# Kernel tuning notes

Measured on AMD Instinct MI355X. Metric: run time of the kernel, lower is better.

The kernel has to match this reference:

```python
import jax, jax.numpy as jnp
import numpy as np

N = 4096          # nodes (single graph, batch=None)
E = 65536         # edges (avg degree 16)
C = 256           # hidden_channels
L = 3             # num_layers
H = 8             # attention heads
EPS = 1e-5        # batchnorm eps


def setup_inputs() -> dict:
    key = jax.random.key(0)
    ks = iter(jax.random.split(key, 64))
    s = 0.05
    d = {}
    d['x'] = jax.random.normal(next(ks), (N, 1), dtype=jnp.float32)
    d['edge_index'] = jax.random.randint(next(ks), (2, E), 0, N, dtype=jnp.int32)
    # input projection Linear(1, C)
    d['lin1_w'] = jax.random.normal(next(ks), (C, 1), dtype=jnp.float32) * s
    d['lin1_b'] = jnp.zeros((C,), dtype=jnp.float32)
    # GIN MLP: Linear(C,C) -> ReLU -> Linear(C,C), stacked over layers
    d['gin_w1'] = jax.random.normal(next(ks), (L, C, C), dtype=jnp.float32) * s
    d['gin_b1'] = jnp.zeros((L, C), dtype=jnp.float32)
    d['gin_w2'] = jax.random.normal(next(ks), (L, C, C), dtype=jnp.float32) * s
    d['gin_b2'] = jnp.zeros((L, C), dtype=jnp.float32)
    # MultiheadAttention projections
    for nm in ['attn_wq', 'attn_wk', 'attn_wv', 'attn_wo']:
        d[nm] = jax.random.normal(next(ks), (L, C, C), dtype=jnp.float32) * s
    for nm in ['attn_bq', 'attn_bk', 'attn_bv', 'attn_bo']:
        d[nm] = jnp.zeros((L, C), dtype=jnp.float32)
    # three BatchNorms per GPSConv layer
    for nm in ['bn1', 'bn2', 'bn3']:
        d[nm + '_g'] = jnp.ones((L, C), dtype=jnp.float32)
        d[nm + '_b'] = jnp.zeros((L, C), dtype=jnp.float32)
    # GPSConv feedforward: Linear(C, 2C) -> ReLU -> Linear(2C, C)
    d['mlp_w1'] = jax.random.normal(next(ks), (L, 2 * C, C), dtype=jnp.float32) * s
    d['mlp_b1'] = jnp.zeros((L, 2 * C), dtype=jnp.float32)
    d['mlp_w2'] = jax.random.normal(next(ks), (L, C, 2 * C), dtype=jnp.float32) * s
    d['mlp_b2'] = jnp.zeros((L, C), dtype=jnp.float32)
    return d


def _bn(v, g, b):
    # training-mode BatchNorm1d over the node dimension (biased variance)
    m = v.mean(0)
    var = v.var(0)
    return (v - m) * jax.lax.rsqrt(var + EPS) * g + b


def _gps_forward(x, edge_index, lin1_w, lin1_b, gin_w1, gin_b1, gin_w2, gin_b2,
                 attn_wq, attn_bq, attn_wk, attn_bk, attn_wv, attn_bv,
                 attn_wo, attn_bo, bn1_g, bn1_b, bn2_g, bn2_b, bn3_g, bn3_b,
                 mlp_w1, mlp_b1, mlp_w2, mlp_b2):
    h = x @ lin1_w.T + lin1_b                     # [N, C]
    src, dst = edge_index[0], edge_index[1]
    dh = C // H
    scale = 1.0 / jnp.sqrt(jnp.float32(dh))
    for l in range(L):
        xin = h
        # --- GIN branch: gather -> scatter-sum -> MLP ---
        agg = jax.ops.segment_sum(xin[src], dst, num_segments=N)   # [N, C]
        z = xin + agg                                               # eps=0
        z = jax.nn.relu(z @ gin_w1[l].T + gin_b1[l]) @ gin_w2[l].T + gin_b2[l]
        h1 = _bn(z + xin, bn1_g[l], bn1_b[l])
        # --- global multihead attention over all N nodes ---
        q = (xin @ attn_wq[l].T + attn_bq[l]).reshape(N, H, dh)
        k = (xin @ attn_wk[l].T + attn_bk[l]).reshape(N, H, dh)
        v = (xin @ attn_wv[l].T + attn_bv[l]).reshape(N, H, dh)
        scores = jnp.einsum('nhd,mhd->hnm', q, k) * scale           # [H, N, N]
        a = jax.nn.softmax(scores, axis=-1)
        o = jnp.einsum('hnm,mhd->nhd', a, v).reshape(N, C)
        o = o @ attn_wo[l].T + attn_bo[l]
        h2 = _bn(o + xin, bn2_g[l], bn2_b[l])
        # --- combine + feedforward ---
        s = h1 + h2
        m = jax.nn.relu(s @ mlp_w1[l].T + mlp_b1[l]) @ mlp_w2[l].T + mlp_b2[l]
        h = _bn(s + m, bn3_g[l], bn3_b[l])
    return h


def reference(x, edge_index, lin1_w, lin1_b, gin_w1, gin_b1, gin_w2, gin_b2,
              attn_wq, attn_bq, attn_wk, attn_bk, attn_wv, attn_bv,
              attn_wo, attn_bo, bn1_g, bn1_b, bn2_g, bn2_b, bn3_g, bn3_b,
              mlp_w1, mlp_b1, mlp_w2, mlp_b2):
    return _gps_forward(x, edge_index, lin1_w, lin1_b, gin_w1, gin_b1, gin_w2,
                        gin_b2, attn_wq, attn_bq, attn_wk, attn_bk, attn_wv,
                        attn_bv, attn_wo, attn_bo, bn1_g, bn1_b, bn2_g, bn2_b,
                        bn3_g, bn3_b, mlp_w1, mlp_b1, mlp_w2, mlp_b2)
```

## Files before the change

### kernel.cpp

```cpp
#include <hip/hip_runtime.h>

#define NN 4096
#define NE 65536
#define C 256
#define NL 3
#define NH 8
#define DH 32
#define EPS 1e-5f
#define SPLIT 4
#define KT8 (NN/128/SPLIT)
#define QB 256
#define ATTN_BLKS ((NN/QB)*NH*SPLIT)
#define VS 136

typedef __bf16 bf16x8 __attribute__((ext_vector_type(8)));
typedef __bf16 bf16x4v __attribute__((ext_vector_type(4)));
typedef float f32x4 __attribute__((ext_vector_type(4)));
typedef short bf16x4s __attribute__((ext_vector_type(4)));

#define QSCALE (0.17677669529663687f * 1.4426950408889634f)

#define CC1 (C*C)
#define GS 72

__global__ __launch_bounds__(256) void prep_w(const float* __restrict__ s0,
        const float* __restrict__ s1, const float* __restrict__ s2,
        const float* __restrict__ s3, const float* __restrict__ s4,
        const float* __restrict__ s5, const float* __restrict__ s6,
        const float* __restrict__ s7, __bf16* __restrict__ dst) {
    int g = blockIdx.y;
    int i = (blockIdx.x*256 + threadIdx.x)*4;
    const float* src; int n;
    switch (g) {
        case 0: src=s0; n=3*CC1; break;
        case 1: src=s1; n=3*CC1; break;
        case 2: src=s2; n=3*CC1; break;
        case 3: src=s3; n=3*CC1; break;
        case 4: src=s4; n=3*CC1; break;
        case 5: src=s5; n=3*CC1; break;
        case 6: src=s6; n=6*CC1; break;
        default: src=s7; n=6*CC1; break;
    }
    if (i >= n) return;
    size_t off;
    if (g >= 2 && g <= 4) {
        int l = i >> 16, rem = i & (CC1-1);
        off = (size_t)(6 + 3*l + (g-2))*CC1 + rem;
    } else {
        size_t base = (g==0) ? 0 : (g==1) ? 3*(size_t)CC1 : (g==5) ? 15*(size_t)CC1
                    : (g==6) ? 18*(size_t)CC1 : 24*(size_t)CC1;
        off = base + i;
    }
    float4 t = *(const float4*)(src + i);
    bf16x4v o = {(__bf16)t.x, (__bf16)t.y, (__bf16)t.z, (__bf16)t.w};
    *(bf16x4v*)(dst + off) = o;
}

__global__ __launch_bounds__(256) void lin1_kernel(const float* __restrict__ x,
        const float* __restrict__ w, const float* __restrict__ b,
        __bf16* __restrict__ out) {
    int n = blockIdx.x, c = threadIdx.x;
    out[(size_t)n*C + c] = (__bf16)(x[n]*w[c] + b[c]);
}

__global__ __launch_bounds__(256) void hist_kernel(const int* __restrict__ ei,
        int* __restrict__ cnt) {
    int e = blockIdx.x*256 + threadIdx.x;
    atomicAdd(&cnt[ei[NE + e]], 1);
}

__global__ __launch_bounds__(256) void scan_kernel(const int* __restrict__ cnt,
        int* __restrict__ rowptr, int* __restrict__ cursor) {
    __shared__ int tot[256];
    __shared__ int pre[257];
    int t = threadIdx.x;
    int base = t*16;
    int local[16];
    int s = 0;
    #pragma unroll
    for (int i = 0; i < 16; i++) { local[i] = s; s += cnt[base+i]; }
    tot[t] = s;
    __syncthreads();
    if (t == 0) {
        int acc = 0;
        for (int i = 0; i < 256; i++) { pre[i] = acc; acc += tot[i]; }
        pre[256] = acc;
    }
    __syncthreads();
    int off = pre[t];
    #pragma unroll
    for (int i = 0; i < 16; i++) {
        rowptr[base+i] = off + local[i];
        cursor[base+i] = off + local[i];
    }
    if (t == 0) rowptr[NN] = pre[256];
}

__global__ __launch_bounds__(256) void fill_kernel(const int* __restrict__ ei,
        int* __restrict__ cursor, int* __restrict__ eidsrc) {
    int e = blockIdx.x*256 + threadIdx.x;
    int dst = ei[NE + e], src = ei[e];
    int pos = atomicAdd(&cursor[dst], 1);
    eidsrc[pos] = src;
}

template<int QKV, int BN, int COMB>
__device__ __forceinline__ void gemm_core(int bm, int bn,
        const __bf16* A, const float* A2f, const __bf16* A2b, const __bf16* W,
        const float* b0, const float* b1, const float* b2,
        const __bf16* add1, const __bf16* add2,
        __bf16* out, __bf16* vt, __bf16* ktp, float* stats,
        const float* coefs,
        const float* st1, const float* g1, const float* bb1,
        const float* st2, const float* g2, const float* bb2,
        const float* lsum,
        int K, int Nout, int relu, __bf16* As, __bf16* Ws) {
    int tid = threadIdx.x;
    int wave = tid >> 6, lane = tid & 63;
    int ln = lane & 15, quad = lane >> 4;
    int row = tid >> 2, kseg = (tid & 3) * 16;
    f32x4 acc[4] = {};
    bf16x8 pa0, pa1, pw0, pw1, pz0, pz1;
    float4 pf0, pf1, pf2, pf3;
    bf16x8 pc0[SPLIT], pc1[SPLIT];
    float pwt[SPLIT];
    auto prefetch = [&](int k0) {
        if constexpr (COMB) {
            int rowg = bm + row;
            int head = (k0 + kseg) >> 5;
            #pragma unroll
            for (int zz = 0; zz < SPLIT; zz++) {
                pwt[zz] = lsum[((size_t)zz*NH + head)*NN + rowg];
                const __bf16* p = &A[((size_t)zz*NN + rowg)*C + k0 + kseg];
                pc0[zz] = *(const bf16x8*)p;
                pc1[zz] = *(const bf16x8*)(p + 8);
            }
        } else {
            const __bf16* ap = &A[(size_t)(bm+row)*K + k0 + kseg];
            pa0 = *(const bf16x8*)ap;
            pa1 = *(const bf16x8*)(ap + 8);
            if constexpr (BN == 1) {
                const __bf16* p = &A2b[(size_t)(bm+row)*K + k0 + kseg];
                pz0 = *(const bf16x8*)p;
                pz1 = *(const bf16x8*)(p + 8);
            } else if (A2f) {
                const float* p = &A2f[(size_t)(bm+row)*K + k0 + kseg];
                pf0 = *(const float4*)p;
                pf1 = *(const float4*)(p+4);
                pf2 = *(const float4*)(p+8);
                pf3 = *(const float4*)(p+12);
            }
        }
        const __bf16* wp = &W[(size_t)(bn+row)*K + k0 + kseg];
        pw0 = *(const bf16x8*)wp;
        pw1 = *(const bf16x8*)(wp + 8);
    };
    prefetch(0);
    for (int k0 = 0; k0 < K; k0 += 64) {
        {
            bf16x8 a0, a1;
            if constexpr (COMB) {
                float tot = 0.f;
                #pragma unroll
                for (int zz = 0; zz < SPLIT; zz++) tot += pwt[zz];
                float inv = 1.0f / tot;
                float v[16] = {};
                #pragma unroll
                for (int zz = 0; zz < SPLIT; zz++) {
                    #pragma unroll
                    for (int j = 0; j < 8; j++) {
                        v[j]   += pwt[zz]*(float)pc0[zz][j];
                        v[8+j] += pwt[zz]*(float)pc1[zz][j];
                    }
                }
                #pragma unroll
                for (int j = 0; j < 8; j++) {
                    a0[j] = (__bf16)(v[j]*inv);
                    a1[j] = (__bf16)(v[8+j]*inv);
                }
            } else {
                a0 = pa0;
                a1 = pa1;
                if constexpr (BN == 1) {
                    float sc1[16], sh1[16], sc2[16], sh2[16];
                    #pragma unroll
                    for (int i = 0; i < 4; i++) {
                        *(float4*)&sc1[i*4] = *(const float4*)&coefs[k0 + kseg + i*4];
                        *(float4*)&sh1[i*4] = *(const float4*)&coefs[C + k0 + kseg + i*4];
                        *(float4*)&sc2[i*4] = *(const float4*)&coefs[2*C + k0 + kseg + i*4];
                        *(float4*)&sh2[i*4] = *(const float4*)&coefs[3*C + k0 + kseg + i*4];
                    }
                    #pragma unroll
                    for (int j = 0; j < 8; j++) {
                        a0[j] = (__bf16)((float)a0[j]*sc1[j] + sh1[j]
                                       + (float)pz0[j]*sc2[j] + sh2[j]);
                        a1[j] = (__bf16)((float)a1[j]*sc1[8+j] + sh1[8+j]
                                       + (float)pz1[j]*sc2[8+j] + sh2[8+j]);
                    }
                } else if (A2f) {
                    a0[0]=(__bf16)((float)a0[0]+pf0.x); a0[1]=(__bf16)((float)a0[1]+pf0.y);
                    a0[2]=(__bf16)((float)a0[2]+pf0.z); a0[3]=(__bf16)((float)a0[3]+pf0.w);
                    a0[4]=(__bf16)((float)a0[4]+pf1.x); a0[5]=(__bf16)((float)a0[5]+pf1.y);
                    a0[6]=(__bf16)((float)a0[6]+pf1.z); a0[7]=(__bf16)((float)a0[7]+pf1.w);
                    a1[0]=(__bf16)((float)a1[0]+pf2.x); a1[1]=(__bf16)((float)a1[1]+pf2.y);
                    a1[2]=(__bf16)((float)a1[2]+pf2.z); a1[3]=(__bf16)((float)a1[3]+pf2.w);
                    a1[4]=(__bf16)((float)a1[4]+pf3.x); a1[5]=(__bf16)((float)a1[5]+pf3.y);
                    a1[6]=(__bf16)((float)a1[6]+pf3.z); a1[7]=(__bf16)((float)a1[7]+pf3.w);
                }
            }
            *(bf16x8*)&As[row*GS + kseg]     = a0;
            *(bf16x8*)&As[row*GS + kseg + 8] = a1;
            *(bf16x8*)&Ws[row*GS + kseg]     = pw0;
            *(bf16x8*)&Ws[row*GS + kseg + 8] = pw1;
        }
        __syncthreads();
        if (k0 + 64 < K) prefetch(k0 + 64);
        #pragma unroll
        for (int kt2 = 0; kt2 < 2; kt2++) {
            bf16x8 bfr = *(const bf16x8*)&Ws[(wave*16+ln)*GS + kt2*32 + quad*8];
            #pragma unroll
            for (int i = 0; i < 4; i++) {
                bf16x8 afr = *(const bf16x8*)&As[(i*16+ln)*GS + kt2*32 + quad*8];
                acc[i] = __builtin_amdgcn_mfma_f32_16x16x32_bf16(afr, bfr, acc[i], 0, 0, 0);
            }
        }
        __syncthreads();
    }
    int col = bn + wave*16 + ln;
    if constexpr (QKV) {
        float bsv = col < 256 ? b0[col] : (col < 512 ? b1[col-256] : b2[col-512]);
        if (col < 256) {
            #pragma unroll
            for (int i = 0; i < 4; i++)
                #pragma unroll
                for (int rr = 0; rr < 4; rr++)
                    out[(size_t)(bm + i*16 + quad*4 + rr)*C + col] =
                        (__bf16)((acc[i][rr] + bsv) * (float)QSCALE);
        } else if (col < 512) {
            int hd = (col-256) >> 5, dh = (col-256) & 31;
            #pragma unroll
            for (int i = 0; i < 4; i++)
                #pragma unroll
                for (int rr = 0; rr < 4; rr++)
                    ktp[((size_t)hd*NN + bm + i*16 + quad*4 + rr)*DH + dh] =
                        (__bf16)(acc[i][rr] + bsv);
        } else {
            int vrow = col - 512;
            #pragma unroll
            for (int i = 0; i < 4; i++) {
                bf16x4v pk = {(__bf16)(acc[i][0]+bsv), (__bf16)(acc[i][1]+bsv),
                              (__bf16)(acc[i][2]+bsv), (__bf16)(acc[i][3]+bsv)};
                *(bf16x4v*)&vt[(size_t)vrow*NN + bm + i*16 + quad*4] = pk;
            }
        }
        return;
    }
    float bsv = b0[col];
    float sc1 = 0.f, sh1 = 0.f, sc2 = 0.f, sh2 = 0.f;
    if constexpr (BN == 2) {
        float m1 = st1[col]*(1.f/NN);
        sc1 = rsqrtf(st1[C+col]*(1.f/NN) - m1*m1 + EPS) * g1[col];
        sh1 = bb1[col] - m1*sc1;
        float m2 = st2[col]*(1.f/NN);
        sc2 = rsqrtf(st2[C+col]*(1.f/NN) - m2*m2 + EPS) * g2[col];
        sh2 = bb2[col] - m2*sc2;
    }
    float ssum = 0.f, ssq = 0.f;
    #pragma unroll
    for (int i = 0; i < 4; i++) {
        #pragma unroll
        for (int rr = 0; rr < 4; rr++) {
            int rw = bm + i*16 + quad*4 + rr;
            float vv = acc[i][rr] + bsv;
            if (relu) vv = fmaxf(vv, 0.f);
            size_t idx = (size_t)rw*Nout + col;
            if constexpr (BN == 2) {
                vv += (float)add1[idx]*sc1 + sh1 + (float)add2[idx]*sc2 + sh2;
            } else {
                if (add1) vv += (float)add1[idx];
                if (add2) vv += (float)add2[idx];
            }
            out[idx] = (__bf16)vv;
            ssum += vv; ssq += vv*vv;
        }
    }
    if (stats) {
        ssum += __shfl_xor(ssum, 16); ssum += __shfl_xor(ssum, 32);
        ssq  += __shfl_xor(ssq, 16);  ssq  += __shfl_xor(ssq, 32);
        if (quad == 0) {
            atomicAdd(&stats[col], ssum);
            atomicAdd(&stats[Nout + col], ssq);
        }
    }
}

__device__ __forceinline__ void attn_body(int t, const __bf16* __restrict__ qbuf,
        const __bf16* __restrict__ kt, const __bf16* __restrict__ vt,
        __bf16* __restrict__ opart, float* __restrict__ lsum, __bf16* lds) {
    int head = t & 7, qi = (t >> 3) & 15, z = t >> 7;
    int qb = qi * QB;
    int hb = head * DH;
    int tid = threadIdx.x;
    int wave = tid >> 6, lane = tid & 63;
    int ln = lane & 15, quad = lane >> 4;
    __bf16* Kb0 = lds;
    __bf16* Kb1 = lds + 4608;
    __bf16* Vb0 = lds + 9216;
    __bf16* Vb1 = lds + 9216 + 32*VS;

    bf16x8 qf[4];
    #pragma unroll
    for (int g = 0; g < 4; g++)
        qf[g] = *(const bf16x8*)&qbuf[(size_t)(qb + wave*64 + g*16 + ln)*C + hb + quad*8];

    f32x4 ot[4][2] = {};
    f32x4 la[4] = {};
    const bf16x4s ones = {(short)0x3F80, (short)0x3F80, (short)0x3F80, (short)0x3F80};
    const f32x4 zz = {0.f,0.f,0.f,0.f};

    int srow = tid >> 1, sseg = (tid & 1) * 16;
    int vd = tid >> 3, vseg = (tid & 7) * 16;
    int kt0 = z * KT8;
    const __bf16* kbase = &kt[(size_t)head*NN*DH];
    {
        int i0 = qi & (KT8-1);
        const __bf16* kp = &kbase[(size_t)((kt0+i0)*128 + srow)*DH + sseg];
        *(bf16x8*)&Kb0[srow*36 + sseg]     = *(const bf16x8*)kp;
        *(bf16x8*)&Kb0[srow*36 + sseg + 8] = *(const bf16x8*)(kp + 8);
        const __bf16* vp = &vt[(size_t)(hb + vd)*NN + (kt0+i0)*128 + vseg];
        *(bf16x8*)&Vb0[vd*VS + vseg]     = *(const bf16x8*)vp;
        *(bf16x8*)&Vb0[vd*VS + vseg + 8] = *(const bf16x8*)(vp + 8);
    }
    for (int ii = 0; ii < KT8; ii++) {
        int inext = (ii + 1 + qi) & (KT8-1);
        __bf16* Kc = (ii & 1) ? Kb1 : Kb0;
        __bf16* Kn = (ii & 1) ? Kb0 : Kb1;
        __bf16* Vc = (ii & 1) ? Vb1 : Vb0;
        __bf16* Vn = (ii & 1) ? Vb0 : Vb1;
        __syncthreads();
        bf16x8 nk0, nk1, nv0, nv1;
        bool hasNext = (ii + 1 < KT8);
        if (hasNext) {
            const __bf16* kp = &kbase[(size_t)((kt0+inext)*128 + srow)*DH + sseg];
            nk0 = *(const bf16x8*)kp;
            nk1 = *(const bf16x8*)(kp + 8);
            const __bf16* vp = &vt[(size_t)(hb + vd)*NN + (kt0+inext)*128 + vseg];
            nv0 = *(const bf16x8*)vp;
            nv1 = *(const bf16x8*)(vp + 8);
        }
        #pragma unroll
        for (int pr = 0; pr < 4; pr++) {
            #pragma unroll
            for (int s = 0; s < 2; s++) {
                int ks = pr*2 + s;
                bf16x8 kf = *(const bf16x8*)&Kc[(ks*16+ln)*36 + quad*8];
                bf16x4s vf0 = *(const bf16x4s*)&Vc[(0*16+ln)*VS + ks*16 + quad*4];
                bf16x4s vf1 = *(const bf16x4s*)&Vc[(1*16+ln)*VS + ks*16 + quad*4];
                f32x4 st0 = __builtin_amdgcn_mfma_f32_16x16x32_bf16(kf, qf[0], zz, 0, 0, 0);
                f32x4 st1 = __builtin_amdgcn_mfma_f32_16x16x32_bf16(kf, qf[1], zz, 0, 0, 0);
                f32x4 st2 = __builtin_amdgcn_mfma_f32_16x16x32_bf16(kf, qf[2], zz, 0, 0, 0);
                f32x4 st3 = __builtin_amdgcn_mfma_f32_16x16x32_bf16(kf, qf[3], zz, 0, 0, 0);
                union { __bf16 b[4]; bf16x4s s; } pf0, pf1, pf2, pf3;
                #pragma unroll
                for (int rr = 0; rr < 4; rr++) {
                    pf0.b[rr] = (__bf16)__builtin_amdgcn_exp2f(st0[rr]);
                    pf1.b[rr] = (__bf16)__builtin_amdgcn_exp2f(st1[rr]);
                    pf2.b[rr] = (__bf16)__builtin_amdgcn_exp2f(st2[rr]);
                    pf3.b[rr] = (__bf16)__builtin_amdgcn_exp2f(st3[rr]);
                }
                ot[0][0] = __builtin_amdgcn_mfma_f32_16x16x16bf16_1k(vf0, pf0.s, ot[0][0], 0, 0, 0);
                ot[0][1] = __builtin_amdgcn_mfma_f32_16x16x16bf16_1k(vf1, pf0.s, ot[0][1], 0, 0, 0);
                ot[1][0] = __builtin_amdgcn_mfma_f32_16x16x16bf16_1k(vf0, pf1.s, ot[1][0], 0, 0, 0);
                ot[1][1] = __builtin_amdgcn_mfma_f32_16x16x16bf16_1k(vf1, pf1.s, ot[1][1], 0, 0, 0);
                ot[2][0] = __builtin_amdgcn_mfma_f32_16x16x16bf16_1k(vf0, pf2.s, ot[2][0], 0, 0, 0);
                ot[2][1] = __builtin_amdgcn_mfma_f32_16x16x16bf16_1k(vf1, pf2.s, ot[2][1], 0, 0, 0);
                ot[3][0] = __builtin_amdgcn_mfma_f32_16x16x16bf16_1k(vf0, pf3.s, ot[3][0], 0, 0, 0);
                ot[3][1] = __builtin_amdgcn_mfma_f32_16x16x16bf16_1k(vf1, pf3.s, ot[3][1], 0, 0, 0);
                la[0]    = __builtin_amdgcn_mfma_f32_16x16x16bf16_1k(ones, pf0.s, la[0], 0, 0, 0);
                la[1]    = __builtin_amdgcn_mfma_f32_16x16x16bf16_1k(ones, pf1.s, la[1], 0, 0, 0);
                la[2]    = __builtin_amdgcn_mfma_f32_16x16x16bf16_1k(ones, pf2.s, la[2], 0, 0, 0);
                la[3]    = __builtin_amdgcn_mfma_f32_16x16x16bf16_1k(ones, pf3.s, la[3], 0, 0, 0);
            }
        }
        if (hasNext) {
            *(bf16x8*)&Kn[srow*36 + sseg]     = nk0;
            *(bf16x8*)&Kn[srow*36 + sseg + 8] = nk1;
            *(bf16x8*)&Vn[vd*VS + vseg]     = nv0;
            *(bf16x8*)&Vn[vd*VS + vseg + 8] = nv1;
        }
    }
    #pragma unroll
    for (int g = 0; g < 4; g++) {
        float l_ = la[g][0];
        float inv = 1.0f / l_;
        int qrow = qb + wave*64 + g*16 + ln;
        #pragma unroll
        for (int h = 0; h < 2; h++) {
            bf16x4v pk = {(__bf16)(ot[g][h][0]*inv), (__bf16)(ot[g][h][1]*inv),
                          (__bf16)(ot[g][h][2]*inv), (__bf16)(ot[g][h][3]*inv)};
            *(bf16x4v*)&opart[((size_t)z*NN + qrow)*C + hb + h*16 + quad*4] = pk;
        }
        if (quad == 0)
            lsum[((size_t)z*NH + head)*NN + qrow] = l_;
    }
}

__global__ __launch_bounds__(256) void qkv_agg_kernel(const __bf16* __restrict__ Hb,
        const __bf16* __restrict__ Wqkv, const float* __restrict__ bq,
        const float* __restrict__ bk, const float* __restrict__ bv,
        __bf16* __restrict__ qout, __bf16* __restrict__ ktout,
        __bf16* __restrict__ vtout,
        const int* __restrict__ rowptr, const int* __restrict__ eidsrc,
        float* __restrict__ agg) {
    __shared__ __bf16 lds[9216];
    int bx = blockIdx.x;
    if (bx < 768) {
        gemm_core<1,0,0>((bx & 63)*64, (bx >> 6)*64, Hb, nullptr, nullptr, Wqkv,
                bq, bk, bv, nullptr, nullptr, qout, vtout, ktout, nullptr,
                nullptr, nullptr, nullptr, nullptr, nullptr, nullptr, nullptr,
                nullptr, C, 768, 0, lds, lds + 4608);
        return;
    }
    int tid = threadIdx.x;
    int wave = tid >> 6, lane = tid & 63;
    int node = (bx - 768)*4 + wave;
    int beg = rowptr[node], end = rowptr[node+1];
    float s0 = 0.f, s1 = 0.f, s2 = 0.f, s3 = 0.f;
    for (int e = beg; e < end; e++) {
        int src = eidsrc[e];
        bf16x4v hv = *(const bf16x4v*)&Hb[(size_t)src*C + lane*4];
        s0 += (float)hv[0]; s1 += (float)hv[1];
        s2 += (float)hv[2]; s3 += (float)hv[3];
    }
    float4 o = {s0, s1, s2, s3};
    *(float4*)&agg[(size_t)node*C + lane*4] = o;
}

__global__ __launch_bounds__(256, 2) void gin1_attn_kernel(const __bf16* __restrict__ Hb,
        const float* __restrict__ agg, const __bf16* __restrict__ gw1,
        const float* __restrict__ gb1, __bf16* __restrict__ t1,
        const __bf16* __restrict__ qbuf, const __bf16* __restrict__ kt,
        const __bf16* __restrict__ vt,
        __bf16* __restrict__ opart, float* __restrict__ lsum) {
    __shared__ __bf16 lds[17920];
    int bx = blockIdx.x;
    if (bx < 256) {
        gemm_core<0,0,0>((bx >> 2)*64, (bx & 3)*64, Hb, agg, nullptr, gw1,
                gb1, nullptr, nullptr, nullptr, nullptr, t1, nullptr, nullptr,
                nullptr, nullptr, nullptr, nullptr, nullptr, nullptr, nullptr,
                nullptr, nullptr, C, C, 1, lds, lds + 4608);
        return;
    }
    attn_body(bx - 256, qbuf, kt, vt, opart, lsum, lds);
}

__global__ __launch_bounds__(256) void gin2_proj_kernel(const __bf16* __restrict__ t1,
        const __bf16* __restrict__ gw2, const float* __restrict__ gb2,
        const __bf16* __restrict__ Hb, __bf16* __restrict__ z1, float* __restrict__ st1,
        const __bf16* __restrict__ opart, const float* __restrict__ lsum,
        const __bf16* __restrict__ wop, const float* __restrict__ lbo,
        __bf16* __restrict__ z2, float* __restrict__ st2) {
    __shared__ __bf16 lds[9216];
    int bx = blockIdx.x;
    if (bx < 256) {
        gemm_core<0,0,0>((bx >> 2)*64, (bx & 3)*64, t1, nullptr, nullptr, gw2,
                gb2, nullptr, nullptr, Hb, nullptr, z1, nullptr, nullptr, st1,
                nullptr, nullptr, nullptr, nullptr, nullptr, nullptr, nullptr,
                nullptr, C, C, 0, lds, lds + 4608);
        return;
    }
    int t = bx - 256;
    gemm_core<0,0,1>((t >> 2)*64, (t & 3)*64, opart, nullptr, nullptr, wop,
            lbo, nullptr, nullptr, Hb, nullptr, z2, nullptr, nullptr, st2,
            nullptr, nullptr, nullptr, nullptr, nullptr, nullptr, nullptr,
            lsum, C, C, 0, lds, lds + 4608);
}

__global__ __launch_bounds__(256) void ff1_kernel(const __bf16* __restrict__ z1,
        const __bf16* __restrict__ z2, const __bf16* __restrict__ mw1,
        const float* __restrict__ lmb1, __bf16* __restrict__ hidden,
        const float* __restrict__ st1, const float* __restrict__ g1,
        const float* __restrict__ bb1, const float* __restrict__ st2,
        const float* __restrict__ g2, const float* __restrict__ bb2) {
    __shared__ __bf16 lds[9216];
    __shared__ float coefs[4*C];
    int tid = threadIdx.x;
    {
        float m = st1[tid]*(1.f/NN);
        float var = st1[C+tid]*(1.f/NN) - m*m;
        float s = rsqrtf(var + EPS) * g1[tid];
        coefs[tid] = s; coefs[C+tid] = bb1[tid] - m*s;
        m = st2[tid]*(1.f/NN);
        var = st2[C+tid]*(1.f/NN) - m*m;
        s = rsqrtf(var + EPS) * g2[tid];
        coefs[2*C+tid] = s; coefs[3*C+tid] = bb2[tid] - m*s;
    }
    __syncthreads();
    int bx = blockIdx.x;
    gemm_core<0,1,0>((bx >> 3)*64, (bx & 7)*64, z1, nullptr, z2, mw1,
            lmb1, nullptr, nullptr, nullptr, nullptr, hidden, nullptr, nullptr,
            nullptr, coefs, nullptr, nullptr, nullptr, nullptr, nullptr, nullptr,
            nullptr, C, 2*C, 1, lds, lds + 4608);
}

__global__ __launch_bounds__(256) void ff2_kernel(const __bf16* __restrict__ hidden,
        const __bf16* __restrict__ mw2, const float* __restrict__ lmb2,
        const __bf16* __restrict__ z1, const __bf16* __restrict__ z2,
        __bf16* __restrict__ zbuf3, float* __restrict__ st3,
        const float* __restrict__ st1, const float* __restrict__ g1,
        const float* __restrict__ bb1, const float* __restrict__ st2,
        const float* __restrict__ g2, const float* __restrict__ bb2) {
    __shared__ __bf16 lds[9216];
    int bx = blockIdx.x;
    gemm_core<0,2,0>((bx >> 2)*64, (bx & 3)*64, hidden, nullptr, nullptr, mw2,
            lmb2, nullptr, nullptr, z1, z2, zbuf3, nullptr, nullptr, st3,
            nullptr, st1, g1, bb1, st2, g2, bb2,
            nullptr, 2*C, C, 0, lds, lds + 4608);
}

__global__ __launch_bounds__(256) void bn_apply_kernel(const __bf16* __restrict__ z,
        const float* __restrict__ stats, const float* __restrict__ g,
        const float* __restrict__ b, __bf16* __restrict__ outb,
        float* __restrict__ outf) {
    int idx4 = (blockIdx.x*256 + threadIdx.x) * 4;
    int c = idx4 & (C-1);
    bf16x4v zv = *(const bf16x4v*)&z[idx4];
    float4 st = *(const float4*)&stats[c];
    float4 sq = *(const float4*)&stats[C + c];
    float4 gv = *(const float4*)&g[c];
    float4 bv = *(const float4*)&b[c];
    float o[4];
    float m0 = st.x*(1.f/NN), m1 = st.y*(1.f/NN), m2 = st.z*(1.f/NN), m3 = st.w*(1.f/NN);
    o[0] = ((float)zv[0] - m0) * rsqrtf(sq.x*(1.f/NN) - m0*m0 + EPS) * gv.x + bv.x;
    o[1] = ((float)zv[1] - m1) * rsqrtf(sq.y*(1.f/NN) - m1*m1 + EPS) * gv.y + bv.y;
    o[2] = ((float)zv[2] - m2) * rsqrtf(sq.z*(1.f/NN) - m2*m2 + EPS) * gv.z + bv.z;
    o[3] = ((float)zv[3] - m3) * rsqrtf(sq.w*(1.f/NN) - m3*m3 + EPS) * gv.w + bv.w;
    if (outb) {
        bf16x4v ov = {(__bf16)o[0], (__bf16)o[1], (__bf16)o[2], (__bf16)o[3]};
        *(bf16x4v*)&outb[idx4] = ov;
    } else {
        float4 ov = {o[0], o[1], o[2], o[3]};
        *(float4*)&outf[idx4] = ov;
    }
}

extern "C" void kernel_launch(void* const* d_in, const int* in_sizes, int n_in,
                              void* d_out, int out_size, void* d_ws, size_t ws_size,
                              hipStream_t stream) {
    const float* x      = (const float*)d_in[0];
    const int*   ei     = (const int*)d_in[1];
    const float* lin1_w = (const float*)d_in[2];
    const float* lin1_b = (const float*)d_in[3];
    const float* gin_w1 = (const float*)d_in[4];
    const float* gin_b1 = (const float*)d_in[5];
    const float* gin_w2 = (const float*)d_in[6];
    const float* gin_b2 = (const float*)d_in[7];
    const float* wq = (const float*)d_in[8];
    const float* wk = (const float*)d_in[9];
    const float* wv = (const float*)d_in[10];
    const float* wo = (const float*)d_in[11];
    const float* bq = (const float*)d_in[12];
    const float* bk = (const float*)d_in[13];
    const float* bv = (const float*)d_in[14];
    const float* bo = (const float*)d_in[15];
    const float* bn1_g = (const float*)d_in[16];
    const float* bn1_b = (const float*)d_in[17];
    const float* bn2_g = (const float*)d_in[18];
    const float* bn2_b = (const float*)d_in[19];
    const float* bn3_g = (const float*)d_in[20];
    const float* bn3_b = (const float*)d_in[21];
    const float* mw1 = (const float*)d_in[22];
    const float* mb1 = (const float*)d_in[23];
    const float* mw2 = (const float*)d_in[24];
    const float* mb2 = (const float*)d_in[25];

    const size_t MB = 1u << 20;
    char* ws = (char*)d_ws;
    __bf16* Hb      = (__bf16*)(ws);
    __bf16* z1      = (__bf16*)(ws + 2*MB);
    __bf16* zbuf3   = (__bf16*)(ws + 4*MB);
    __bf16* z2      = (__bf16*)(ws + 6*MB);
    __bf16* t1      = (__bf16*)(ws + 8*MB);
    __bf16* Qbuf    = (__bf16*)(ws + 10*MB);
    __bf16* Ktb     = (__bf16*)(ws + 12*MB);
    __bf16* Vt      = (__bf16*)(ws + 14*MB);
    float*  agg     = (float*)(ws + 16*MB);
    __bf16* hiddenb = (__bf16*)(ws + 16*MB);
    __bf16* Opart   = (__bf16*)(ws + 20*MB);
    __bf16* Wb      = (__bf16*)(ws + 28*MB);
    float*  stats   = (float*)(ws + 32*MB);
    int*    cursor  = (int*)(ws + 32*MB + 64*1024);
    int*    rowptr  = (int*)(ws + 32*MB + 96*1024);
    int*    eidsrc  = (int*)(ws + 32*MB + 128*1024);
    float*  lsum    = (float*)(ws + 33*MB);

    dim3 blk(256);

    prep_w<<<dim3(384, 8), blk, 0, stream>>>(gin_w1, gin_w2, wq, wk, wv, wo, mw1, mw2, Wb);
    hipMemsetAsync(stats, 0, 9 * 2 * C * sizeof(float), stream);
    lin1_kernel<<<NN, blk, 0, stream>>>(x, lin1_w, lin1_b, Hb);
    hipMemsetAsync(cursor, 0, NN * sizeof(int), stream);
    hist_kernel<<<NE/256, blk, 0, stream>>>(ei, cursor);
    scan_kernel<<<1, blk, 0, stream>>>(cursor, rowptr, cursor);
    fill_kernel<<<NE/256, blk, 0, stream>>>(ei, cursor, eidsrc);

    for (int l = 0; l < NL; l++) {
        const __bf16* gw1b = Wb + (size_t)l*CC1;
        const __bf16* gw2b = Wb + (size_t)(3+l)*CC1;
        const __bf16* wqkv = Wb + (size_t)(6+3*l)*CC1;
        const __bf16* wop  = Wb + (size_t)(15+l)*CC1;
        const __bf16* mw1p = Wb + (size_t)(18+2*l)*CC1;
        const __bf16* mw2p = Wb + (size_t)(24+2*l)*CC1;
        const float* gb1 = gin_b1 + (size_t)l*C;
        const float* gb2 = gin_b2 + (size_t)l*C;
        const float* lbq = bq + (size_t)l*C;
        const float* lbk = bk + (size_t)l*C;
        const float* lbv = bv + (size_t)l*C;
        const float* lbo = bo + (size_t)l*C;
        const float* lmb1 = mb1 + (size_t)l*2*C;
        const float* lmb2 = mb2 + (size_t)l*C;
        float* st1 = stats + (size_t)l*3*2*C;
        float* st2 = st1 + 2*C;
        float* st3 = st2 + 2*C;
        const float* g1v = bn1_g + (size_t)l*C; const float* b1v = bn1_b + (size_t)l*C;
        const float* g2v = bn2_g + (size_t)l*C; const float* b2v = bn2_b + (size_t)l*C;

        qkv_agg_kernel<<<768 + NN/4, blk, 0, stream>>>(Hb, wqkv, lbq, lbk, lbv,
                Qbuf, Ktb, Vt, rowptr, eidsrc, agg);
        gin1_attn_kernel<<<256 + ATTN_BLKS, blk, 0, stream>>>(Hb, agg,
                gw1b, gb1, t1, Qbuf, Ktb, Vt, Opart, lsum);
        gin2_proj_kernel<<<512, blk, 0, stream>>>(t1, gw2b, gb2, Hb, z1, st1,
                Opart, lsum, wop, lbo, z2, st2);
        ff1_kernel<<<512, blk, 0, stream>>>(z1, z2, mw1p, lmb1, hiddenb,
                st1, g1v, b1v, st2, g2v, b2v);
        ff2_kernel<<<256, blk, 0, stream>>>(hiddenb, mw2p, lmb2, z1, z2,
                zbuf3, st3, st1, g1v, b1v, st2, g2v, b2v);
        if (l == NL-1)
            bn_apply_kernel<<<NN/4, blk, 0, stream>>>(zbuf3, st3,
                    bn3_g + (size_t)l*C, bn3_b + (size_t)l*C, nullptr, (float*)d_out);
        else
            bn_apply_kernel<<<NN/4, blk, 0, stream>>>(zbuf3, st3,
                    bn3_g + (size_t)l*C, bn3_b + (size_t)l*C, Hb, nullptr);
    }
}
```

Baseline: 391.2 us.

## Fold previous layer's BatchNorm3 into next layer's consumers and halve attention split

Removes the intermediate bn_apply launch between layers. Each consumer kernel (the QKV GEMM, neighbour aggregation, GIN1 GEMM, and the residual adds in GIN2 and the output projection) now applies the previous layer's BN3 scale and shift on the fly from raw zbuf3 plus stats. This saves one full read/write pass over the node features per layer and one kernel launch. The attention key split is also lowered from 4 to 2, which halves the partial-output combine work but also halves the number of attention blocks. That costs parallelism, and the per-consumer affine math adds ALU work and per-block coefficient setup.

Result: slower. 414.4 us (+5.9%).

```diff
diff --git a/kernel.cpp b/kernel.cpp
--- a/kernel.cpp
+++ b/kernel.cpp
@@ -7,11 +7,11 @@
 #define NH 8
 #define DH 32
 #define EPS 1e-5f
-#define SPLIT 4
+#define SPLIT 2
 #define KT8 (NN/128/SPLIT)
 #define QB 256
+#define VS 136
 #define ATTN_BLKS ((NN/QB)*NH*SPLIT)
-#define VS 136
 
 typedef __bf16 bf16x8 __attribute__((ext_vector_type(8)));
 typedef __bf16 bf16x4v __attribute__((ext_vector_type(4)));
@@ -104,7 +104,7 @@
     eidsrc[pos] = src;
 }
 
-template<int QKV, int BN, int COMB>
+template<int QKV, int BN, int COMB, int AAF>
 __device__ __forceinline__ void gemm_core(int bm, int bn,
         const __bf16* A, const float* A2f, const __bf16* A2b, const __bf16* W,
         const float* b0, const float* b1, const float* b2,
@@ -114,6 +114,8 @@
         const float* st1, const float* g1, const float* bb1,
         const float* st2, const float* g2, const float* bb2,
         const float* lsum,
+        const float* acoefs,
+        const float* rst3, const float* rg3, const float* rb3,
         int K, int Nout, int relu, __bf16* As, __bf16* Ws) {
     int tid = threadIdx.x;
     int wave = tid >> 6, lane = tid & 63;
@@ -181,6 +183,19 @@
             } else {
                 a0 = pa0;
                 a1 = pa1;
+                if constexpr (AAF) {
+                    float asc[16], ash[16];
+                    #pragma unroll
+                    for (int i = 0; i < 4; i++) {
+                        *(float4*)&asc[i*4] = *(const float4*)&acoefs[k0 + kseg + i*4];
+                        *(float4*)&ash[i*4] = *(const float4*)&acoefs[C + k0 + kseg + i*4];
+                    }
+                    #pragma unroll
+                    for (int j = 0; j < 8; j++) {
+                        a0[j] = (__bf16)((float)a0[j]*asc[j] + ash[j]);
+                        a1[j] = (__bf16)((float)a1[j]*asc[8+j] + ash[8+j]);
+                    }
+                }
                 if constexpr (BN == 1) {
                     float sc1[16], sh1[16], sc2[16], sh2[16];
                     #pragma unroll
@@ -265,6 +280,12 @@
         sc2 = rsqrtf(st2[C+col]*(1.f/NN) - m2*m2 + EPS) * g2[col];
         sh2 = bb2[col] - m2*sc2;
     }
+    float r1sc = 1.f, r1sh = 0.f;
+    if (rst3) {
+        float m3 = rst3[col]*(1.f/NN);
+        r1sc = rsqrtf(rst3[C+col]*(1.f/NN) - m3*m3 + EPS) * rg3[col];
+        r1sh = rb3[col] - m3*r1sc;
+    }
     float ssum = 0.f, ssq = 0.f;
     #pragma unroll
     for (int i = 0; i < 4; i++) {
@@ -277,7 +298,10 @@
             if constexpr (BN == 2) {
                 vv += (float)add1[idx]*sc1 + sh1 + (float)add2[idx]*sc2 + sh2;
             } else {
-                if (add1) vv += (float)add1[idx];
+                if (add1) {
+                    float t1v = (float)add1[idx];
+                    vv += rst3 ? (t1v*r1sc + r1sh) : t1v;
+                }
                 if (add2) vv += (float)add2[idx];
             }
             out[idx] = (__bf16)vv;
@@ -405,50 +429,75 @@
     }
 }
 
-__global__ __launch_bounds__(256) void qkv_agg_kernel(const __bf16* __restrict__ Hb,
+__global__ __launch_bounds__(256) void qkv_agg_kernel(const __bf16* __restrict__ srcH,
         const __bf16* __restrict__ Wqkv, const float* __restrict__ bq,
         const float* __restrict__ bk, const float* __restrict__ bv,
         __bf16* __restrict__ qout, __bf16* __restrict__ ktout,
         __bf16* __restrict__ vtout,
         const int* __restrict__ rowptr, const int* __restrict__ eidsrc,
-        float* __restrict__ agg) {
+        float* __restrict__ agg,
+        const float* __restrict__ st3p, const float* __restrict__ g3p,
+        const float* __restrict__ b3p) {
     __shared__ __bf16 lds[9216];
+    __shared__ float coefs[2*C];
+    int tid = threadIdx.x;
+    if (st3p) {
+        float m = st3p[tid]*(1.f/NN);
+        float sc = rsqrtf(st3p[C+tid]*(1.f/NN) - m*m + EPS) * g3p[tid];
+        coefs[tid] = sc; coefs[C+tid] = b3p[tid] - m*sc;
+    } else { coefs[tid] = 1.f; coefs[C+tid] = 0.f; }
+    __syncthreads();
     int bx = blockIdx.x;
     if (bx < 768) {
-        gemm_core<1,0,0>((bx & 63)*64, (bx >> 6)*64, Hb, nullptr, nullptr, Wqkv,
+        gemm_core<1,0,0,1>((bx & 63)*64, (bx >> 6)*64, srcH, nullptr, nullptr, Wqkv,
                 bq, bk, bv, nullptr, nullptr, qout, vtout, ktout, nullptr,
                 nullptr, nullptr, nullptr, nullptr, nullptr, nullptr, nullptr,
-                nullptr, C, 768, 0, lds, lds + 4608);
+                nullptr, coefs, nullptr, nullptr, nullptr,
+                C, 768, 0, lds, lds + 4608);
         return;
     }
-    int tid = threadIdx.x;
     int wave = tid >> 6, lane = tid & 63;
+    float4 sc4 = *(const float4*)&coefs[lane*4];
+    float4 sh4 = *(const float4*)&coefs[C + lane*4];
     int node = (bx - 768)*4 + wave;
     int beg = rowptr[node], end = rowptr[node+1];
     float s0 = 0.f, s1 = 0.f, s2 = 0.f, s3 = 0.f;
     for (int e = beg; e < end; e++) {
         int src = eidsrc[e];
-        bf16x4v hv = *(const bf16x4v*)&Hb[(size_t)src*C + lane*4];
-        s0 += (float)hv[0]; s1 += (float)hv[1];
-        s2 += (float)hv[2]; s3 += (float)hv[3];
+        bf16x4v hv = *(const bf16x4v*)&srcH[(size_t)src*C + lane*4];
+        s0 += sc4.x*(float)hv[0] + sh4.x;
+        s1 += sc4.y*(float)hv[1] + sh4.y;
+        s2 += sc4.z*(float)hv[2] + sh4.z;
+        s3 += sc4.w*(float)hv[3] + sh4.w;
     }
     float4 o = {s0, s1, s2, s3};
     *(float4*)&agg[(size_t)node*C + lane*4] = o;
 }
 
-__global__ __launch_bounds__(256, 2) void gin1_attn_kernel(const __bf16* __restrict__ Hb,
+__global__ __launch_bounds__(256, 2) void gin1_attn_kernel(const __bf16* __restrict__ srcH,
         const float* __restrict__ agg, const __bf16* __restrict__ gw1,
         const float* __restrict__ gb1, __bf16* __restrict__ t1,
         const __bf16* __restrict__ qbuf, const __bf16* __restrict__ kt,
         const __bf16* __restrict__ vt,
-        __bf16* __restrict__ opart, float* __restrict__ lsum) {
+        __bf16* __restrict__ opart, float* __restrict__ lsum,
+        const float* __restrict__ st3p, const float* __restrict__ g3p,
+        const float* __restrict__ b3p) {
     __shared__ __bf16 lds[17920];
+    __shared__ float coefs[2*C];
+    int tid = threadIdx.x;
+    if (st3p) {
+        float m = st3p[tid]*(1.f/NN);
+        float sc = rsqrtf(st3p[C+tid]*(1.f/NN) - m*m + EPS) * g3p[tid];
+        coefs[tid] = sc; coefs[C+tid] = b3p[tid] - m*sc;
+    } else { coefs[tid] = 1.f; coefs[C+tid] = 0.f; }
+    __syncthreads();
     int bx = blockIdx.x;
     if (bx < 256) {
-        gemm_core<0,0,0>((bx >> 2)*64, (bx & 3)*64, Hb, agg, nullptr, gw1,
+        gemm_core<0,0,0,1>((bx >> 2)*64, (bx & 3)*64, srcH, agg, nullptr, gw1,
                 gb1, nullptr, nullptr, nullptr, nullptr, t1, nullptr, nullptr,
                 nullptr, nullptr, nullptr, nullptr, nullptr, nullptr, nullptr,
-                nullptr, nullptr, C, C, 1, lds, lds + 4608);
+                nullptr, nullptr, coefs, nullptr, nullptr, nullptr,
+                C, C, 1, lds, lds + 4608);
         return;
     }
     attn_body(bx - 256, qbuf, kt, vt, opart, lsum, lds);
@@ -456,24 +505,28 @@
 
 __global__ __launch_bounds__(256) void gin2_proj_kernel(const __bf16* __restrict__ t1,
         const __bf16* __restrict__ gw2, const float* __restrict__ gb2,
-        const __bf16* __restrict__ Hb, __bf16* __restrict__ z1, float* __restrict__ st1,
+        const __bf16* __restrict__ srcH, __bf16* __restrict__ z1, float* __restrict__ st1,
         const __bf16* __restrict__ opart, const float* __restrict__ lsum,
         const __bf16* __restrict__ wop, const float* __restrict__ lbo,
-        __bf16* __restrict__ z2, float* __restrict__ st2) {
+        __bf16* __restrict__ z2, float* __restrict__ st2,
+        const float* __restrict__ st3p, const float* __restrict__ g3p,
+        const float* __restrict__ b3p) {
     __shared__ __bf16 lds[9216];
     int bx = blockIdx.x;
     if (bx < 256) {
-        gemm_core<0,0,0>((bx >> 2)*64, (bx & 3)*64, t1, nullptr, nullptr, gw2,
-                gb2, nullptr, nullptr, Hb, nullptr, z1, nullptr, nullptr, st1,
+        gemm_core<0,0,0,0>((bx >> 2)*64, (bx & 3)*64, t1, nullptr, nullptr, gw2,
+                gb2, nullptr, nullptr, srcH, nullptr, z1, nullptr, nullptr, st1,
                 nullptr, nullptr, nullptr, nullptr, nullptr, nullptr, nullptr,
-                nullptr, C, C, 0, lds, lds + 4608);
+                nullptr, nullptr, st3p, g3p, b3p,
+                C, C, 0, lds, lds + 4608);
         return;
     }
     int t = bx - 256;
-    gemm_core<0,0,1>((t >> 2)*64, (t & 3)*64, opart, nullptr, nullptr, wop,
-            lbo, nullptr, nullptr, Hb, nullptr, z2, nullptr, nullptr, st2,
+    gemm_core<0,0,1,0>((t >> 2)*64, (t & 3)*64, opart, nullptr, nullptr, wop,
+            lbo, nullptr, nullptr, srcH, nullptr, z2, nullptr, nullptr, st2,
             nullptr, nullptr, nullptr, nullptr, nullptr, nullptr, nullptr,
-            lsum, C, C, 0, lds, lds + 4608);
+            lsum, nullptr, st3p, g3p, b3p,
+            C, C, 0, lds, lds + 4608);
 }
 
 __global__ __launch_bounds__(256) void ff1_kernel(const __bf16* __restrict__ z1,
@@ -497,10 +550,11 @@
     }
     __syncthreads();
     int bx = blockIdx.x;
-    gemm_core<0,1,0>((bx >> 3)*64, (bx & 7)*64, z1, nullptr, z2, mw1,
+    gemm_core<0,1,0,0>((bx >> 3)*64, (bx & 7)*64, z1, nullptr, z2, mw1,
             lmb1, nullptr, nullptr, nullptr, nullptr, hidden, nullptr, nullptr,
             nullptr, coefs, nullptr, nullptr, nullptr, nullptr, nullptr, nullptr,
-            nullptr, C, 2*C, 1, lds, lds + 4608);
+            nullptr, nullptr, nullptr, nullptr, nullptr,
+            C, 2*C, 1, lds, lds + 4608);
 }
 
 __global__ __launch_bounds__(256) void ff2_kernel(const __bf16* __restrict__ hidden,
@@ -512,16 +566,16 @@
         const float* __restrict__ g2, const float* __restrict__ bb2) {
     __shared__ __bf16 lds[9216];
     int bx = blockIdx.x;
-    gemm_core<0,2,0>((bx >> 2)*64, (bx & 3)*64, hidden, nullptr, nullptr, mw2,
+    gemm_core<0,2,0,0>((bx >> 2)*64, (bx & 3)*64, hidden, nullptr, nullptr, mw2,
             lmb2, nullptr, nullptr, z1, z2, zbuf3, nullptr, nullptr, st3,
             nullptr, st1, g1, bb1, st2, g2, bb2,
-            nullptr, 2*C, C, 0, lds, lds + 4608);
+            nullptr, nullptr, nullptr, nullptr, nullptr,
+            2*C, C, 0, lds, lds + 4608);
 }
 
 __global__ __launch_bounds__(256) void bn_apply_kernel(const __bf16* __restrict__ z,
         const float* __restrict__ stats, const float* __restrict__ g,
-        const float* __restrict__ b, __bf16* __restrict__ outb,
-        float* __restrict__ outf) {
+        const float* __restrict__ b, float* __restrict__ outf) {
     int idx4 = (blockIdx.x*256 + threadIdx.x) * 4;
     int c = idx4 & (C-1);
     bf16x4v zv = *(const bf16x4v*)&z[idx4];
@@ -535,13 +589,8 @@
     o[1] = ((float)zv[1] - m1) * rsqrtf(sq.y*(1.f/NN) - m1*m1 + EPS) * gv.y + bv.y;
     o[2] = ((float)zv[2] - m2) * rsqrtf(sq.z*(1.f/NN) - m2*m2 + EPS) * gv.z + bv.z;
     o[3] = ((float)zv[3] - m3) * rsqrtf(sq.w*(1.f/NN) - m3*m3 + EPS) * gv.w + bv.w;
-    if (outb) {
-        bf16x4v ov = {(__bf16)o[0], (__bf16)o[1], (__bf16)o[2], (__bf16)o[3]};
-        *(bf16x4v*)&outb[idx4] = ov;
-    } else {
-        float4 ov = {o[0], o[1], o[2], o[3]};
-        *(float4*)&outf[idx4] = ov;
-    }
+    float4 ov = {o[0], o[1], o[2], o[3]};
+    *(float4*)&outf[idx4] = ov;
 }
 
 extern "C" void kernel_launch(void* const* d_in, const int* in_sizes, int n_in,
@@ -625,21 +674,23 @@
         const float* g1v = bn1_g + (size_t)l*C; const float* b1v = bn1_b + (size_t)l*C;
         const float* g2v = bn2_g + (size_t)l*C; const float* b2v = bn2_b + (size_t)l*C;
 
-        qkv_agg_kernel<<<768 + NN/4, blk, 0, stream>>>(Hb, wqkv, lbq, lbk, lbv,
-                Qbuf, Ktb, Vt, rowptr, eidsrc, agg);
-        gin1_attn_kernel<<<256 + ATTN_BLKS, blk, 0, stream>>>(Hb, agg,
-                gw1b, gb1, t1, Qbuf, Ktb, Vt, Opart, lsum);
-        gin2_proj_kernel<<<512, blk, 0, stream>>>(t1, gw2b, gb2, Hb, z1, st1,
-                Opart, lsum, wop, lbo, z2, st2);
+        const __bf16* srcH = (l == 0) ? Hb : zbuf3;
+        const float* st3p = (l == 0) ? nullptr : stats + (size_t)(l-1)*3*2*C + 4*C;
+        const float* g3p  = (l == 0) ? nullptr : bn3_g + (size_t)(l-1)*C;
+        const float* b3p  = (l == 0) ? nullptr : bn3_b + (size_t)(l-1)*C;
+
+        qkv_agg_kernel<<<768 + NN/4, blk, 0, stream>>>(srcH, wqkv, lbq, lbk, lbv,
+                Qbuf, Ktb, Vt, rowptr, eidsrc, agg, st3p, g3p, b3p);
+        gin1_attn_kernel<<<256 + ATTN_BLKS, blk, 0, stream>>>(srcH, agg,
+                gw1b, gb1, t1, Qbuf, Ktb, Vt, Opart, lsum, st3p, g3p, b3p);
+        gin2_proj_kernel<<<512, blk, 0, stream>>>(t1, gw2b, gb2, srcH, z1, st1,
+                Opart, lsum, wop, lbo, z2, st2, st3p, g3p, b3p);
         ff1_kernel<<<512, blk, 0, stream>>>(z1, z2, mw1p, lmb1, hiddenb,
                 st1, g1v, b1v, st2, g2v, b2v);
         ff2_kernel<<<256, blk, 0, stream>>>(hiddenb, mw2p, lmb2, z1, z2,
                 zbuf3, st3, st1, g1v, b1v, st2, g2v, b2v);
         if (l == NL-1)
             bn_apply_kernel<<<NN/4, blk, 0, stream>>>(zbuf3, st3,
-                    bn3_g + (size_t)l*C, bn3_b + (size_t)l*C, nullptr, (float*)d_out);
-        else
-            bn_apply_kernel<<<NN/4, blk, 0, stream>>>(zbuf3, st3,
-                    bn3_g + (size_t)l*C, bn3_b + (size_t)l*C, Hb, nullptr);
-    }
-}
+                    bn3_g + (size_t)l*C, bn3_b + (size_t)l*C, (float*)d_out);
+    }
+}
```
